# Optimization experiments

Hardware: AMD Instinct MI355X
Metric: run time of the kernel (lower is better)

Reference implementation:

```python
import jax, jax.numpy as jnp
import numpy as np

N, D, R, E = 50000, 256, 4, 800000
LN_EPS = 1e-5
NEG_INF = -1e30  # finite stand-in for -inf so softmax stays grad-safe


def _layernorm(x, g, b):
    m = x.mean(axis=-1, keepdims=True)
    v = x.var(axis=-1, keepdims=True)
    return (x - m) / jnp.sqrt(v + LN_EPS) * g + b


def setup_inputs() -> dict:
    key = jax.random.key(0)
    ks = jax.random.split(key, 8)
    s = 1.0 / np.sqrt(D).astype(np.float32)
    return {
        'rows': jax.random.randint(ks[0], (R, E), 0, N),
        'cols': jax.random.randint(ks[1], (R, E), 0, N),
        'vals': jax.random.uniform(ks[2], (R, E), jnp.float32),
        'node_emb': jax.random.normal(ks[3], (N, D), jnp.float32) * s,
        'pre_W': jax.random.normal(ks[4], (D, D), jnp.float32) * s,
        'pre_b': jnp.zeros((D,), jnp.float32),
        'ln1_g': jnp.ones((D,), jnp.float32),
        'ln1_b': jnp.zeros((D,), jnp.float32),
        'rel_W': jax.random.normal(ks[5], (R, D, D), jnp.float32) * s,
        'attn_vec': jax.random.normal(ks[6], (D,), jnp.float32) * s,
        'self_W': jax.random.normal(ks[7], (D, D), jnp.float32) * s,
        'self_b': jnp.zeros((D,), jnp.float32),
        'bias': jnp.zeros((D,), jnp.float32),
        'ln2_g': jnp.ones((D,), jnp.float32),
        'ln2_b': jnp.zeros((D,), jnp.float32),
    }


def reference(rows, cols, vals, node_emb, pre_W, pre_b, ln1_g, ln1_b, rel_W,
              attn_vec, self_W, self_b, bias, ln2_g, ln2_b):
    # active_indices = arange(N), so x_all is the full embedding table
    x_all = node_emb
    # pre_encoder: Linear -> LayerNorm -> GELU (exact erf, torch default)
    x = jax.nn.gelu(_layernorm(x_all @ pre_W + pre_b, ln1_g, ln1_b), approximate=False)
    # per-relation: relation linear then SpMM (adj_t @ x_rel) via gather + segment_sum
    msgs = []
    for i in range(R):
        x_rel = x @ rel_W[i]                              # [N, D]
        contrib = vals[i][:, None] * x_rel[cols[i]]       # [E, D]
        msgs.append(jax.ops.segment_sum(contrib, rows[i], num_segments=N))
    stacked = jnp.stack(msgs, axis=1)                     # [N, R, D]
    # semantic attention over relations
    scores = jnp.einsum('nrd,d->nr', stacked, attn_vec)   # [N, R]
    mask = jnp.any(stacked != 0, axis=2)                  # [N, R]
    attn = jax.nn.softmax(jnp.where(mask, scores, NEG_INF), axis=1)
    attn = attn * mask                                    # == nan_to_num(softmax(-inf rows))
    out = jnp.einsum('nrd,nr->nd', stacked, attn) + bias + (x @ self_W + self_b)
    out = jax.nn.gelu(out, approximate=False)
    # active_indices = arange(N): scatter into global index space is identity
    final = _layernorm(out, ln2_g, ln2_b)
    return final, attn, x_all
```

## Files before the change

kernel.cpp:

```cpp
#include <hip/hip_runtime.h>
#include <hip/hip_fp16.h>
#include <math.h>


typedef __attribute__((ext_vector_type(8))) short bf16x8;
typedef __attribute__((ext_vector_type(4))) float f32x4;
typedef __attribute__((ext_vector_type(4))) unsigned u32x4;
typedef unsigned long long u64;

__device__ __forceinline__ float gelu_exact(float v) {
    return 0.5f * v * (1.0f + erff(v * 0.70710678118654752f));
}
__device__ __forceinline__ unsigned short f2bf(float f) {
    unsigned u = __float_as_uint(f);
    return (unsigned short)((u + 0x7fffu + ((u >> 16) & 1u)) >> 16);
}
__device__ __forceinline__ unsigned pack2(float a, float b) {
    return (unsigned)f2bf(a) | ((unsigned)f2bf(b) << 16);
}
__device__ __forceinline__ unsigned short f2h(float f) {
    return __half_as_ushort(__float2half(f));
}
__device__ __forceinline__ __half2 u2h2(unsigned u) {
    union { unsigned u; __half2 h; } c; c.u = u; return c.h;
}
__device__ __forceinline__ void gload16(const void* g, void* l) {
    __builtin_amdgcn_global_load_lds(
        (const __attribute__((address_space(1))) void*)g,
        (__attribute__((address_space(3))) void*)l, 16, 0, 0);
}

__global__ __launch_bounds__(256)
void conv_emb(const float* __restrict__ ne, unsigned short* __restrict__ emb,
              float* __restrict__ outX, int total4)
{
    const int stride = gridDim.x * blockDim.x;
    for (int i = blockIdx.x * blockDim.x + threadIdx.x; i < total4; i += stride) {
        const float4 v = reinterpret_cast<const float4*>(ne)[i];
        reinterpret_cast<float4*>(outX)[i] = v;
        ushort4 h;
        h.x = f2bf(v.x); h.y = f2bf(v.y); h.z = f2bf(v.z); h.w = f2bf(v.w);
        reinterpret_cast<ushort4*>(emb)[i] = h;
    }
}

__global__ __launch_bounds__(256)
void build_bt(const float* __restrict__ relW, const float* __restrict__ selfW,
              const float* __restrict__ preW, unsigned short* __restrict__ BTm,
              unsigned short* __restrict__ BTp)
{
    const int idx = blockIdx.x * 256 + threadIdx.x;
    if (idx < 1280 * 256) {
        const int k = idx >> 8, n = idx & 255;
        const float v = (k < 1024)
            ? relW[(size_t)(k >> 8) * 65536 + (size_t)(k & 255) * 256 + n]
            : selfW[(size_t)(k - 1024) * 256 + n];
        BTm[(size_t)n * 1280 + k] = f2bf(v);
    } else {
        const int i2 = idx - 1280 * 256;
        if (i2 < 256 * 256) {
            const int k = i2 >> 8, n = i2 & 255;
            BTp[(size_t)n * 256 + k] = f2bf(preW[(size_t)k * 256 + n]);
        }
    }
}

template<int MODE>
__global__ __launch_bounds__(512)
void gemm_mfma(const unsigned short* __restrict__ a0,
               const unsigned short* __restrict__ a1,
               const unsigned short* __restrict__ a2,
               const unsigned short* __restrict__ a3,
               const unsigned short* __restrict__ a4,
               const unsigned short* __restrict__ BT,
               const float* __restrict__ bias0, const float* __restrict__ bias1,
               const float* __restrict__ lng, const float* __restrict__ lnb,
               float* __restrict__ Cout, unsigned short* __restrict__ XOut,
               unsigned short* __restrict__ XH, int M)
{
    constexpr int K    = MODE ? 1280 : 256;
    constexpr int NSEG = MODE ? 5 : 1;

    __shared__ __align__(16) unsigned char smA[128 * 128];
    __shared__ __align__(16) unsigned char smB[256 * 128];
    __shared__ float redS[4][128];
    __shared__ float redQ[4][128];

    const int tid = threadIdx.x;
    const int w   = tid >> 6;
    const int l   = tid & 63;
    const int wm  = w >> 2, wn = w & 3;
    const int brow = blockIdx.x * 128;

    const int srow = l >> 3;
    const int sgA  = (l & 7) ^ srow;

    f32x4 acc[4][4];
#pragma unroll
    for (int mb = 0; mb < 4; ++mb)
#pragma unroll
        for (int nb = 0; nb < 4; ++nb)
            acc[mb][nb] = f32x4{0.f, 0.f, 0.f, 0.f};

    for (int seg = 0; seg < NSEG; ++seg) {
        const unsigned short* Abase =
            (MODE == 0) ? a0
                        : (seg == 0 ? a0 : seg == 1 ? a1 : seg == 2 ? a2
                                         : seg == 3 ? a3 : a4);
#pragma unroll
        for (int kk = 0; kk < 4; ++kk) {
            __syncthreads();
#pragma unroll
            for (int c = 0; c < 2; ++c) {
                const int r0 = (w * 2 + c) * 8;
                int gm = brow + r0 + srow;
                gm = min(gm, M - 1);
                gload16(Abase + ((size_t)gm << 8) + kk * 64 + sgA * 8,
                        smA + (w * 2 + c) * 1024);
            }
#pragma unroll
            for (int c = 0; c < 4; ++c) {
                const int bn = (w * 4 + c) * 8 + srow;
                gload16(BT + (size_t)bn * K + (seg * 4 + kk) * 64 + sgA * 8,
                        smB + (w * 4 + c) * 1024);
            }
            __syncthreads();

#pragma unroll
            for (int ks = 0; ks < 2; ++ks) {
                bf16x8 af[4], bf[4];
#pragma unroll
                for (int mb = 0; mb < 4; ++mb) {
                    const int row = wm * 64 + mb * 16 + (l & 15);
                    const int g   = (ks * 4 + (l >> 4)) ^ (row & 7);
                    af[mb] = *reinterpret_cast<const bf16x8*>(smA + row * 128 + g * 16);
                }
#pragma unroll
                for (int nb = 0; nb < 4; ++nb) {
                    const int row = wn * 64 + nb * 16 + (l & 15);
                    const int g   = (ks * 4 + (l >> 4)) ^ (row & 7);
                    bf[nb] = *reinterpret_cast<const bf16x8*>(smB + row * 128 + g * 16);
                }
#pragma unroll
                for (int mb = 0; mb < 4; ++mb)
#pragma unroll
                    for (int nb = 0; nb < 4; ++nb)
                        acc[mb][nb] = __builtin_amdgcn_mfma_f32_16x16x32_bf16(
                            af[mb], bf[nb], acc[mb][nb], 0, 0, 0);
            }
        }
    }

    float bb[4], gw[4], bw[4];
#pragma unroll
    for (int nb = 0; nb < 4; ++nb) {
        const int n = wn * 64 + nb * 16 + (l & 15);
        bb[nb] = bias0[n] + (MODE == 1 ? bias1[n] : 0.0f);
        gw[nb] = lng[n];
        bw[nb] = lnb[n];
    }
#pragma unroll
    for (int mb = 0; mb < 4; ++mb)
#pragma unroll
        for (int nb = 0; nb < 4; ++nb)
#pragma unroll
            for (int rg = 0; rg < 4; ++rg) {
                float v = acc[mb][nb][rg] + bb[nb];
                if (MODE == 1) v = gelu_exact(v);
                acc[mb][nb][rg] = v;
            }
#pragma unroll
    for (int mb = 0; mb < 4; ++mb)
#pragma unroll
        for (int rg = 0; rg < 4; ++rg) {
            float s = 0.f, q = 0.f;
#pragma unroll
            for (int nb = 0; nb < 4; ++nb) {
                const float v = acc[mb][nb][rg];
                s += v; q += v * v;
            }
#pragma unroll
            for (int off = 1; off < 16; off <<= 1) {
                s += __shfl_xor(s, off, 64);
                q += __shfl_xor(q, off, 64);
            }
            if ((l & 15) == 0) {
                const int row = wm * 64 + mb * 16 + (l >> 4) * 4 + rg;
                redS[wn][row] = s;
                redQ[wn][row] = q;
            }
        }
    __syncthreads();
    if (tid < 128) {
        const float s = redS[0][tid] + redS[1][tid] + redS[2][tid] + redS[3][tid];
        const float q = redQ[0][tid] + redQ[1][tid] + redQ[2][tid] + redQ[3][tid];
        const float mean = s * (1.0f / 256.0f);
        const float var  = q * (1.0f / 256.0f) - mean * mean;
        redS[0][tid] = mean;
        redQ[0][tid] = rsqrtf(var + 1e-5f);
    }
    __syncthreads();
#pragma unroll
    for (int mb = 0; mb < 4; ++mb)
#pragma unroll
        for (int rg = 0; rg < 4; ++rg) {
            const int row = wm * 64 + mb * 16 + (l >> 4) * 4 + rg;
            if (brow + row >= M) continue;
            const float mu = redS[0][row];
            const float rs = redQ[0][row];
#pragma unroll
            for (int nb = 0; nb < 4; ++nb) {
                const int n = wn * 64 + nb * 16 + (l & 15);
                const float v = (acc[mb][nb][rg] - mu) * rs * gw[nb] + bw[nb];
                if (MODE == 0) {
                    const float gv = gelu_exact(v);
                    XOut[((size_t)(brow + row) << 8) + n] = f2bf(gv);
                    XH[((size_t)(brow + row) << 8) + n]   = f2h(gv);
                } else {
                    Cout[((size_t)(brow + row) << 8) + n] = v;
                }
            }
        }
}

__global__ __launch_bounds__(256)
void wtilde_kernel(const float* __restrict__ relW, const float* __restrict__ av,
                   float* __restrict__ wt)
{
    __shared__ float avs[256];
    const int r = blockIdx.x, tid = threadIdx.x;
    avs[tid] = av[tid];
    __syncthreads();
    const float* W = relW + (size_t)r * 65536 + (size_t)tid * 256;
    float s = 0.f;
    for (int j = 0; j < 256; j += 4) {
        const float4 w4 = *reinterpret_cast<const float4*>(W + j);
        s += w4.x * avs[j] + w4.y * avs[j + 1] + w4.z * avs[j + 2] + w4.w * avs[j + 3];
    }
    wt[r * 256 + tid] = s;
}

__global__ __launch_bounds__(256)
void y_kernel(const unsigned short* __restrict__ XB, const float* __restrict__ wt,
              float* __restrict__ y, int Nn)
{
    const int n = blockIdx.x * 4 + (threadIdx.x >> 6);
    if (n >= Nn) return;
    const int l = threadIdx.x & 63;
    const uint2 d = *reinterpret_cast<const uint2*>(XB + ((size_t)n << 8) + l * 4);
    float xv[4];
    xv[0] = __uint_as_float(d.x << 16);
    xv[1] = __uint_as_float(d.x & 0xffff0000u);
    xv[2] = __uint_as_float(d.y << 16);
    xv[3] = __uint_as_float(d.y & 0xffff0000u);
    float s[4];
#pragma unroll
    for (int r = 0; r < 4; ++r) {
        const float4 w4 = *reinterpret_cast<const float4*>(wt + r * 256 + l * 4);
        s[r] = xv[0] * w4.x + xv[1] * w4.y + xv[2] * w4.z + xv[3] * w4.w;
#pragma unroll
        for (int off = 32; off; off >>= 1) s[r] += __shfl_xor(s[r], off, 64);
    }
    if (l == 0)
        *reinterpret_cast<float4*>(y + (size_t)n * 4) = make_float4(s[0], s[1], s[2], s[3]);
}

__global__ __launch_bounds__(256)
void hist_bin(const int* __restrict__ rows, int* __restrict__ cnt_t,
              int RE, int E, int Nn, int chunk, int NBIN)
{
    __shared__ int lh[800];
    const int blk = blockIdx.x;
    for (int i = threadIdx.x; i < NBIN; i += 256) lh[i] = 0;
    __syncthreads();
    const int e0 = blk * chunk;
    const int e1 = min(e0 + chunk, RE);
    for (int e = e0 + threadIdx.x; e < e1; e += 256) {
        const int r   = e / E;
        const int wid = r * Nn + rows[e];
        atomicAdd(&lh[wid >> 8], 1);
    }
    __syncthreads();
    for (int i = threadIdx.x; i < NBIN; i += 256)
        cnt_t[i * gridDim.x + blk] = lh[i];
}

__global__ __launch_bounds__(256)
void scan_blocks(const int* __restrict__ counts, int* __restrict__ offs,
                 int* __restrict__ bsums, int n)
{
    __shared__ int sh[256];
    const int t = threadIdx.x;
    const int base = blockIdx.x * 1024 + t * 4;
    int v[4], s = 0;
#pragma unroll
    for (int j = 0; j < 4; ++j) {
        v[j] = (base + j < n) ? counts[base + j] : 0;
        s += v[j];
    }
    sh[t] = s;
    __syncthreads();
    for (int off = 1; off < 256; off <<= 1) {
        const int x = (t >= off) ? sh[t - off] : 0;
        __syncthreads();
        sh[t] += x;
        __syncthreads();
    }
    int run = sh[t] - s;
    if (t == 255) bsums[blockIdx.x] = sh[255];
#pragma unroll
    for (int j = 0; j < 4; ++j) {
        if (base + j < n) offs[base + j] = run;
        run += v[j];
    }
}

__global__ __launch_bounds__(256)
void scan_bsums(int* __restrict__ bsums, int nblk)
{
    __shared__ int sh[256];
    const int t = threadIdx.x;
    const int v = (t < nblk) ? bsums[t] : 0;
    sh[t] = v;
    __syncthreads();
    for (int off = 1; off < 256; off <<= 1) {
        const int x = (t >= off) ? sh[t - off] : 0;
        __syncthreads();
        sh[t] += x;
        __syncthreads();
    }
    if (t < nblk) bsums[t] = sh[t] - v;
}

__global__ __launch_bounds__(256)
void scan_add(int* __restrict__ offs, const int* __restrict__ bsums, int n)
{
    const int i = blockIdx.x * 256 + threadIdx.x;
    if (i >= n) return;
    offs[i] += bsums[i >> 10];
}

__global__ __launch_bounds__(256)
void scatter_coarse(const int* __restrict__ rows, const int* __restrict__ cols,
                    const float* __restrict__ vals, const int* __restrict__ ctoffs,
                    u64* __restrict__ edc, int RE, int E, int Nn,
                    int chunk, int NBIN)
{
    __shared__ int lcur[800];
    const int blk = blockIdx.x;
    for (int i = threadIdx.x; i < NBIN; i += 256)
        lcur[i] = ctoffs[i * gridDim.x + blk];
    __syncthreads();
    const int e0 = blk * chunk;
    const int e1 = min(e0 + chunk, RE);
    for (int e = e0 + threadIdx.x; e < e1; e += 256) {
        const int r   = e / E;
        const int row = rows[e];
        const int wid = r * Nn + row;
        const int pos = atomicAdd(&lcur[wid >> 8], 1);
        const unsigned vb = __float_as_uint(vals[e]);
        edc[pos] = ((u64)((vb & 0xFFFFFFFCu) | (unsigned)r) << 32)
                 | ((unsigned)row << 16) | (unsigned)cols[e];
    }
}

__global__ __launch_bounds__(256)
void scatter_fine(const u64* __restrict__ edc, const int* __restrict__ ctoffs,
                  int* __restrict__ offs, u64* __restrict__ edata,
                  int RE, int Nn, int NB1, int NBIN)
{
    __shared__ int cnt[256];
    __shared__ int cur[256];
    const int bin     = blockIdx.x;
    const int widbase = bin << 8;
    const int RN      = Nn << 2;
    const int t       = threadIdx.x;
    cnt[t] = 0;
    __syncthreads();
    const int cs = ctoffs[bin * NB1];
    const int ce = (bin + 1 < NBIN) ? ctoffs[(bin + 1) * NB1] : RE;
    for (int j = cs + t; j < ce; j += 256) {
        const u64 p = edc[j];
        const unsigned hi = (unsigned)(p >> 32);
        const unsigned lo = (unsigned)p;
        const int w = (int)(hi & 3u) * Nn + (int)(lo >> 16);
        atomicAdd(&cnt[w - widbase], 1);
    }
    __syncthreads();
    const int v = cnt[t];
    cur[t] = v;
    __syncthreads();
    for (int off = 1; off < 256; off <<= 1) {
        const int x = (t >= off) ? cur[t - off] : 0;
        __syncthreads();
        cur[t] += x;
        __syncthreads();
    }
    const int excl = cur[t] - v;
    const int wid  = widbase + t;
    if (wid < RN) offs[wid] = cs + excl;
    __syncthreads();
    cur[t] = cs + excl;
    __syncthreads();
    for (int j = cs + t; j < ce; j += 256) {
        const u64 p  = edc[j];
        const unsigned hi = (unsigned)(p >> 32);
        const unsigned lo = (unsigned)p;
        const int w   = (int)(hi & 3u) * Nn + (int)(lo >> 16);
        const int pos = atomicAdd(&cur[w - widbase], 1);
        edata[pos] = ((u64)(hi & 0xFFFFFFFCu) << 32) | (lo & 0xFFFFu);
    }
}

__global__ __launch_bounds__(256)
void score_csr(const int* __restrict__ offs, const u64* __restrict__ edata,
               const float* __restrict__ y, float* __restrict__ scores,
               int Nn, int RE)
{
    const int wid = blockIdx.x * 256 + threadIdx.x;
    const int RN  = Nn << 2;
    if (wid >= RN) return;
    const int r = wid / Nn;
    const int n = wid - r * Nn;
    const int start = offs[wid];
    const int end   = (wid + 1 < RN) ? offs[wid + 1] : RE;

    float s = 0.f;
    int j = start;
    for (; j + 3 < end; j += 4) {
        u64 e[4];
        float yv[4], vv[4];
#pragma unroll
        for (int q = 0; q < 4; ++q) e[q] = __builtin_nontemporal_load(edata + j + q);
#pragma unroll
        for (int q = 0; q < 4; ++q) {
            vv[q] = __uint_as_float((unsigned)(e[q] >> 32));
            yv[q] = y[((size_t)(unsigned)(e[q] & 0xffffffffu)) * 4 + r];
        }
#pragma unroll
        for (int q = 0; q < 4; ++q) s = fmaf(vv[q], yv[q], s);
    }
    for (; j < end; ++j) {
        const u64 e0 = edata[j];
        s = fmaf(__uint_as_float((unsigned)(e0 >> 32)),
                 y[((size_t)(unsigned)(e0 & 0xffffffffu)) * 4 + r], s);
    }
    scores[(size_t)n * 4 + r] = (end > start) ? s : -1e30f;
}

__global__ __launch_bounds__(256)
void softmax4(const float* __restrict__ scores, float* __restrict__ attn, int Nn)
{
    const int n = blockIdx.x * 256 + threadIdx.x;
    if (n >= Nn) return;
    const float4 s4 = *reinterpret_cast<const float4*>(scores + (size_t)n * 4);
    float s[4] = { s4.x, s4.y, s4.z, s4.w };
    float mx = -3.0e38f;
#pragma unroll
    for (int r = 0; r < 4; ++r) mx = fmaxf(mx, s[r]);
    float ex[4], es = 0.f;
#pragma unroll
    for (int r = 0; r < 4; ++r) { ex[r] = expf(s[r] - mx); es += ex[r]; }
    const float inv = 1.0f / es;
    float4 o;
    o.x = (s[0] > -1e29f) ? ex[0] * inv : 0.0f;
    o.y = (s[1] > -1e29f) ? ex[1] * inv : 0.0f;
    o.z = (s[2] > -1e29f) ? ex[2] * inv : 0.0f;
    o.w = (s[3] > -1e29f) ? ex[3] * inv : 0.0f;
    *reinterpret_cast<float4*>(attn + (size_t)n * 4) = o;
}

__global__ __launch_bounds__(256)
void agg_csr(const int* __restrict__ offs, const u64* __restrict__ edata,
             const unsigned short* __restrict__ xh, const float* __restrict__ attn,
             unsigned short* __restrict__ agg, int Nn, int RE)
{
    const int wid  = (blockIdx.x << 2) + (threadIdx.x >> 6);
    const int lane = threadIdx.x & 63;
    const int half = lane >> 5;
    const int sub  = lane & 31;
    const int RN   = Nn << 2;
    if (wid >= RN) return;
    const int r = wid / Nn;
    const int n = wid - r * Nn;

    const int start = offs[wid];
    const int end   = (wid + 1 < RN) ? offs[wid + 1] : RE;

    __half2 acc0 = __float2half2_rn(0.f), acc1 = acc0, acc2 = acc0, acc3 = acc0;

    int j = start + half;
    for (; j + 2 < end; j += 4) {
        const u64 e0 = __builtin_nontemporal_load(edata + j);
        const u64 e1 = __builtin_nontemporal_load(edata + j + 2);
        const int c0 = (int)(e0 & 0xffffffffu);
        const int c1 = (int)(e1 & 0xffffffffu);
        const __half2 v0 = __float2half2_rn(__uint_as_float((unsigned)(e0 >> 32)));
        const __half2 v1 = __float2half2_rn(__uint_as_float((unsigned)(e1 >> 32)));
        const uint4 d0 = *reinterpret_cast<const uint4*>(xh + ((size_t)c0 << 8) + sub * 8);
        const uint4 d1 = *reinterpret_cast<const uint4*>(xh + ((size_t)c1 << 8) + sub * 8);
        acc0 = __hfma2(v0, u2h2(d0.x), acc0);
        acc1 = __hfma2(v0, u2h2(d0.y), acc1);
        acc2 = __hfma2(v0, u2h2(d0.z), acc2);
        acc3 = __hfma2(v0, u2h2(d0.w), acc3);
        acc0 = __hfma2(v1, u2h2(d1.x), acc0);
        acc1 = __hfma2(v1, u2h2(d1.y), acc1);
        acc2 = __hfma2(v1, u2h2(d1.z), acc2);
        acc3 = __hfma2(v1, u2h2(d1.w), acc3);
    }
    for (; j < end; j += 2) {
        const u64 e0 = __builtin_nontemporal_load(edata + j);
        const int c0 = (int)(e0 & 0xffffffffu);
        const __half2 v0 = __float2half2_rn(__uint_as_float((unsigned)(e0 >> 32)));
        const uint4 d0 = *reinterpret_cast<const uint4*>(xh + ((size_t)c0 << 8) + sub * 8);
        acc0 = __hfma2(v0, u2h2(d0.x), acc0);
        acc1 = __hfma2(v0, u2h2(d0.y), acc1);
        acc2 = __hfma2(v0, u2h2(d0.z), acc2);
        acc3 = __hfma2(v0, u2h2(d0.w), acc3);
    }

    float a[8];
    a[0] = __low2float(acc0); a[1] = __high2float(acc0);
    a[2] = __low2float(acc1); a[3] = __high2float(acc1);
    a[4] = __low2float(acc2); a[5] = __high2float(acc2);
    a[6] = __low2float(acc3); a[7] = __high2float(acc3);
#pragma unroll
    for (int i = 0; i < 8; ++i) a[i] += __shfl_xor(a[i], 32, 64);

    if (half == 0) {
        const float sc = attn[(size_t)n * 4 + r];
        u32x4 st;
        st.x = pack2(sc * a[0], sc * a[1]);
        st.y = pack2(sc * a[2], sc * a[3]);
        st.z = pack2(sc * a[4], sc * a[5]);
        st.w = pack2(sc * a[6], sc * a[7]);
        __builtin_nontemporal_store(
            st, reinterpret_cast<u32x4*>(agg + ((size_t)wid << 8) + sub * 8));
    }
}

extern "C" void kernel_launch(void* const* d_in, const int* in_sizes, int n_in,
                              void* d_out, int out_size, void* d_ws, size_t ws_size,
                              hipStream_t stream)
{
    const int*   rows     = (const int*)d_in[0];
    const int*   cols     = (const int*)d_in[1];
    const float* vals     = (const float*)d_in[2];
    const float* node_emb = (const float*)d_in[3];
    const float* pre_W    = (const float*)d_in[4];
    const float* pre_b    = (const float*)d_in[5];
    const float* ln1_g    = (const float*)d_in[6];
    const float* ln1_b    = (const float*)d_in[7];
    const float* rel_W    = (const float*)d_in[8];
    const float* attn_vec = (const float*)d_in[9];
    const float* self_W   = (const float*)d_in[10];
    const float* self_b   = (const float*)d_in[11];
    const float* bias     = (const float*)d_in[12];
    const float* ln2_g    = (const float*)d_in[13];
    const float* ln2_b    = (const float*)d_in[14];

    const int Dd = 256;
    const int R  = in_sizes[8] / (Dd * Dd);
    const int N  = in_sizes[3] / Dd;
    const int E  = in_sizes[0] / R;
    const int RE = R * E;
    const int RN = R * N;

    const int NB1   = 256;
    const int chunk = (RE + NB1 - 1) / NB1;
    const int NBIN  = (RN + 255) / 256;
    const int NCT   = NBIN * NB1;

    float* out  = (float*)d_out;
    float* outF = out;
    float* outA = out + (size_t)N * Dd;
    float* outX = outA + (size_t)N * R;

    char* wp = (char*)d_ws;
    auto alloc = [&](size_t bytes) {
        char* p = wp;
        wp += (bytes + 255) & ~(size_t)255;
        return p;
    };
    unsigned short* AGGS = (unsigned short*)alloc((size_t)RN * Dd * 2);
    unsigned short* XB   = (unsigned short*)alloc((size_t)N * Dd * 2);
    unsigned short* XH   = (unsigned short*)alloc((size_t)N * Dd * 2);
    unsigned short* EMB  = (unsigned short*)alloc((size_t)N * Dd * 2);
    unsigned short* BTm  = (unsigned short*)alloc((size_t)Dd * 1280 * 2);
    unsigned short* BTp  = (unsigned short*)alloc((size_t)Dd * Dd * 2);
    float* WT   = (float*)alloc((size_t)R * Dd * 4);
    float* Y    = (float*)alloc((size_t)N * R * 4);
    float* SC   = (float*)alloc((size_t)N * R * 4);
    int* offs   = (int*)alloc((size_t)RN * 4);
    int* cnt_t  = (int*)alloc((size_t)NCT * 4);
    int* ctoffs = cnt_t;
    int* bsums2 = (int*)alloc(1024);
    u64* edata  = (u64*)alloc((size_t)RE * 8);
    u64* edc    = (u64*)alloc((size_t)RE * 8);

    const int gblocks = (N + 127) / 128;
    const int nblkC   = (NCT + 1023) / 1024;

    build_bt<<<(1280 * 256 + 256 * 256 + 255) / 256, 256, 0, stream>>>(
        rel_W, self_W, pre_W, BTm, BTp);
    conv_emb<<<2048, 256, 0, stream>>>(node_emb, EMB, outX, N * Dd / 4);

    gemm_mfma<0><<<gblocks, 512, 0, stream>>>(EMB, nullptr, nullptr, nullptr, nullptr,
                                              BTp, pre_b, nullptr, ln1_g, ln1_b,
                                              nullptr, XB, XH, N);
    wtilde_kernel<<<R, 256, 0, stream>>>(rel_W, attn_vec, WT);
    y_kernel<<<(N + 3) / 4, 256, 0, stream>>>(XB, WT, Y, N);

    hist_bin<<<NB1, 256, 0, stream>>>(rows, cnt_t, RE, E, N, chunk, NBIN);
    scan_blocks<<<nblkC, 256, 0, stream>>>(cnt_t, ctoffs, bsums2, NCT);
    scan_bsums<<<1, 256, 0, stream>>>(bsums2, nblkC);
    scan_add<<<(NCT + 255) / 256, 256, 0, stream>>>(ctoffs, bsums2, NCT);
    scatter_coarse<<<NB1, 256, 0, stream>>>(rows, cols, vals, ctoffs, edc,
                                            RE, E, N, chunk, NBIN);
    scatter_fine<<<NBIN, 256, 0, stream>>>(edc, ctoffs, offs, edata, RE, N, NB1, NBIN);

    score_csr<<<(RN + 255) / 256, 256, 0, stream>>>(offs, edata, Y, SC, N, RE);
    softmax4<<<(N + 255) / 256, 256, 0, stream>>>(SC, outA, N);

    agg_csr<<<(RN + 3) / 4, 256, 0, stream>>>(offs, edata, XH, outA, AGGS, N, RE);

    gemm_mfma<1><<<gblocks, 512, 0, stream>>>(AGGS, AGGS + (size_t)N * Dd,
                                              AGGS + (size_t)2 * N * Dd,
                                              AGGS + (size_t)3 * N * Dd, XB,
                                              BTm, bias, self_b, ln2_g, ln2_b,
                                              outF, nullptr, nullptr, N);
}
```

Before: 589.3 us.

## Fuse attention score computation into CSR scatter and unroll aggregation loop

Removes the separate score_csr kernel by accumulating val*y[col] per (relation,row) slot with shared-memory float atomics inside scatter_fine, while the edge is already in registers. This saves one launch and a full extra pass over edata plus y gathers. Separately, the agg_csr inner loop is unrolled to four edges per half-wave to put more gather loads in flight. Shared float atomics make the score summation order nondeterministic, and the deeper unroll raises register pressure.

Result: faster. 560.0 us (-5.0%).

```diff
diff --git a/kernel.cpp b/kernel.cpp
--- a/kernel.cpp
+++ b/kernel.cpp
@@ -367,15 +367,18 @@
 __global__ __launch_bounds__(256)
 void scatter_fine(const u64* __restrict__ edc, const int* __restrict__ ctoffs,
                   int* __restrict__ offs, u64* __restrict__ edata,
+                  const float* __restrict__ y, float* __restrict__ SC,
                   int RE, int Nn, int NB1, int NBIN)
 {
-    __shared__ int cnt[256];
-    __shared__ int cur[256];
+    __shared__ int   cnt[256];
+    __shared__ int   cur[256];
+    __shared__ float scr[256];
     const int bin     = blockIdx.x;
     const int widbase = bin << 8;
     const int RN      = Nn << 2;
     const int t       = threadIdx.x;
     cnt[t] = 0;
+    scr[t] = 0.f;
     __syncthreads();
     const int cs = ctoffs[bin * NB1];
     const int ce = (bin + 1 < NBIN) ? ctoffs[(bin + 1) * NB1] : RE;
@@ -406,46 +409,20 @@
         const u64 p  = edc[j];
         const unsigned hi = (unsigned)(p >> 32);
         const unsigned lo = (unsigned)p;
-        const int w   = (int)(hi & 3u) * Nn + (int)(lo >> 16);
+        const int r   = (int)(hi & 3u);
+        const int col = (int)(lo & 0xFFFFu);
+        const int w   = r * Nn + (int)(lo >> 16);
         const int pos = atomicAdd(&cur[w - widbase], 1);
-        edata[pos] = ((u64)(hi & 0xFFFFFFFCu) << 32) | (lo & 0xFFFFu);
-    }
-}
-
-__global__ __launch_bounds__(256)
-void score_csr(const int* __restrict__ offs, const u64* __restrict__ edata,
-               const float* __restrict__ y, float* __restrict__ scores,
-               int Nn, int RE)
-{
-    const int wid = blockIdx.x * 256 + threadIdx.x;
-    const int RN  = Nn << 2;
-    if (wid >= RN) return;
-    const int r = wid / Nn;
-    const int n = wid - r * Nn;
-    const int start = offs[wid];
-    const int end   = (wid + 1 < RN) ? offs[wid + 1] : RE;
-
-    float s = 0.f;
-    int j = start;
-    for (; j + 3 < end; j += 4) {
-        u64 e[4];
-        float yv[4], vv[4];
-#pragma unroll
-        for (int q = 0; q < 4; ++q) e[q] = __builtin_nontemporal_load(edata + j + q);
-#pragma unroll
-        for (int q = 0; q < 4; ++q) {
-            vv[q] = __uint_as_float((unsigned)(e[q] >> 32));
-            yv[q] = y[((size_t)(unsigned)(e[q] & 0xffffffffu)) * 4 + r];
-        }
-#pragma unroll
-        for (int q = 0; q < 4; ++q) s = fmaf(vv[q], yv[q], s);
-    }
-    for (; j < end; ++j) {
-        const u64 e0 = edata[j];
-        s = fmaf(__uint_as_float((unsigned)(e0 >> 32)),
-                 y[((size_t)(unsigned)(e0 & 0xffffffffu)) * 4 + r], s);
-    }
-    scores[(size_t)n * 4 + r] = (end > start) ? s : -1e30f;
+        edata[pos] = ((u64)(hi & 0xFFFFFFFCu) << 32) | (unsigned)col;
+        const float val = __uint_as_float(hi & 0xFFFFFFFCu);
+        atomicAdd(&scr[w - widbase], val * y[(size_t)col * 4 + r]);
+    }
+    __syncthreads();
+    if (wid < RN) {
+        const int r = wid / Nn;
+        const int n = wid - r * Nn;
+        SC[(size_t)n * 4 + r] = (v > 0) ? scr[t] : -1e30f;
+    }
 }
 
 __global__ __launch_bounds__(256)
@@ -490,23 +467,26 @@
     __half2 acc0 = __float2half2_rn(0.f), acc1 = acc0, acc2 = acc0, acc3 = acc0;
 
     int j = start + half;
-    for (; j + 2 < end; j += 4) {
-        const u64 e0 = __builtin_nontemporal_load(edata + j);
-        const u64 e1 = __builtin_nontemporal_load(edata + j + 2);
-        const int c0 = (int)(e0 & 0xffffffffu);
-        const int c1 = (int)(e1 & 0xffffffffu);
-        const __half2 v0 = __float2half2_rn(__uint_as_float((unsigned)(e0 >> 32)));
-        const __half2 v1 = __float2half2_rn(__uint_as_float((unsigned)(e1 >> 32)));
-        const uint4 d0 = *reinterpret_cast<const uint4*>(xh + ((size_t)c0 << 8) + sub * 8);
-        const uint4 d1 = *reinterpret_cast<const uint4*>(xh + ((size_t)c1 << 8) + sub * 8);
-        acc0 = __hfma2(v0, u2h2(d0.x), acc0);
-        acc1 = __hfma2(v0, u2h2(d0.y), acc1);
-        acc2 = __hfma2(v0, u2h2(d0.z), acc2);
-        acc3 = __hfma2(v0, u2h2(d0.w), acc3);
-        acc0 = __hfma2(v1, u2h2(d1.x), acc0);
-        acc1 = __hfma2(v1, u2h2(d1.y), acc1);
-        acc2 = __hfma2(v1, u2h2(d1.z), acc2);
-        acc3 = __hfma2(v1, u2h2(d1.w), acc3);
+    for (; j + 6 < end; j += 8) {
+        u64 e[4];
+#pragma unroll
+        for (int q = 0; q < 4; ++q)
+            e[q] = __builtin_nontemporal_load(edata + j + 2 * q);
+        uint4 d[4];
+        __half2 vv[4];
+#pragma unroll
+        for (int q = 0; q < 4; ++q) {
+            const int c = (int)(e[q] & 0xffffffffu);
+            vv[q] = __float2half2_rn(__uint_as_float((unsigned)(e[q] >> 32)));
+            d[q]  = *reinterpret_cast<const uint4*>(xh + ((size_t)c << 8) + sub * 8);
+        }
+#pragma unroll
+        for (int q = 0; q < 4; ++q) {
+            acc0 = __hfma2(vv[q], u2h2(d[q].x), acc0);
+            acc1 = __hfma2(vv[q], u2h2(d[q].y), acc1);
+            acc2 = __hfma2(vv[q], u2h2(d[q].z), acc2);
+            acc3 = __hfma2(vv[q], u2h2(d[q].w), acc3);
+        }
     }
     for (; j < end; j += 2) {
         const u64 e0 = __builtin_nontemporal_load(edata + j);
@@ -617,9 +597,9 @@
     scan_add<<<(NCT + 255) / 256, 256, 0, stream>>>(ctoffs, bsums2, NCT);
     scatter_coarse<<<NB1, 256, 0, stream>>>(rows, cols, vals, ctoffs, edc,
                                             RE, E, N, chunk, NBIN);
-    scatter_fine<<<NBIN, 256, 0, stream>>>(edc, ctoffs, offs, edata, RE, N, NB1, NBIN);
-
-    score_csr<<<(RN + 255) / 256, 256, 0, stream>>>(offs, edata, Y, SC, N, RE);
+    scatter_fine<<<NBIN, 256, 0, stream>>>(edc, ctoffs, offs, edata, Y, SC,
+                                           RE, N, NB1, NBIN);
+
     softmax4<<<(N + 255) / 256, 256, 0, stream>>>(SC, outA, N);
 
     agg_csr<<<(RN + 3) / 4, 256, 0, stream>>>(offs, edata, XH, outA, AGGS, N, RE);
```
